# Kernel tuning notes

Measured on AMD Instinct MI355X. Metric: run time of the kernel, lower is better.

## Reference

```python
import jax, jax.numpy as jnp
import numpy as np

B, T, D, H = 2, 2048, 1024, 16
DK = D // H


def setup_inputs() -> dict:
    key = jax.random.key(0)
    ks = jax.random.split(key, 9)
    s = 1.0 / np.sqrt(D)
    x = jax.random.normal(ks[0], (B, T, D), dtype=jnp.float32)
    # causal mask (1 = attend, 0 = masked), broadcast over batch and heads
    mask = jnp.tril(jnp.ones((T, T), dtype=jnp.int32))[None, None, :, :]
    Wq = jax.random.uniform(ks[1], (D, D), jnp.float32, -s, s)
    bq = jax.random.uniform(ks[2], (D,), jnp.float32, -s, s)
    Wk = jax.random.uniform(ks[3], (D, D), jnp.float32, -s, s)
    bk = jax.random.uniform(ks[4], (D,), jnp.float32, -s, s)
    Wv = jax.random.uniform(ks[5], (D, D), jnp.float32, -s, s)
    bv = jax.random.uniform(ks[6], (D,), jnp.float32, -s, s)
    Wo = jax.random.uniform(ks[7], (D, D), jnp.float32, -s, s)
    bo = jax.random.uniform(ks[8], (D,), jnp.float32, -s, s)
    return {"x": x, "mask": mask, "Wq": Wq, "bq": bq, "Wk": Wk, "bk": bk,
            "Wv": Wv, "bv": bv, "Wo": Wo, "bo": bo}


def reference(x, mask, Wq, bq, Wk, bk, Wv, bv, Wo, bo):
    # nn.Linear: y = x @ W.T + b
    q = (x @ Wq.T + bq).reshape(B, T, H, DK).transpose(0, 2, 1, 3)  # [B,H,T,DK]
    k = (x @ Wk.T + bk).reshape(B, T, H, DK).transpose(0, 2, 1, 3)
    v = (x @ Wv.T + bv).reshape(B, T, H, DK).transpose(0, 2, 1, 3)
    scores = jnp.einsum('bhqd,bhkd->bhqk', q, k) / np.sqrt(DK).astype(np.float32)
    scores = jnp.where(mask == 0, -jnp.inf, scores)
    attn = jax.nn.softmax(scores, axis=-1)
    out = jnp.einsum('bhqk,bhkd->bhqd', attn, v)  # [B,H,T,DK]
    out = out.transpose(0, 2, 1, 3).reshape(B, T, D)
    return out @ Wo.T + bo
```

## Files before the change

kernel.cpp:

```cpp
#include <hip/hip_runtime.h>

typedef unsigned short u16;
typedef unsigned int u32;
typedef unsigned long long u64;
typedef __attribute__((ext_vector_type(8))) short short8;
typedef __attribute__((ext_vector_type(4))) float f32x4;

#define B_ 2
#define T_ 2048
#define H_ 16
#define DK_ 64
#define QSCALE 0.18033688011112042f

__device__ __forceinline__ u16 f2bf(float f){
  unsigned u = __float_as_uint(f);
  return (u16)((u + 0x7fffu + ((u >> 16) & 1u)) >> 16);
}

__device__ __forceinline__ u32 cvtpk(float lo, float hi){
  u32 r;
  asm("v_cvt_pk_bf16_f32 %0, %1, %2" : "=v"(r) : "v"(lo), "v"(hi));
  return r;
}

__device__ __forceinline__ short8 pack8(const f32x4 a, const f32x4 b){
  union { u32 u[4]; short8 s; } t;
  t.u[0] = cvtpk(a[0], a[1]); t.u[1] = cvtpk(a[2], a[3]);
  t.u[2] = cvtpk(b[0], b[1]); t.u[3] = cvtpk(b[2], b[3]);
  return t.s;
}

#define EXP2(x) __builtin_exp2f(x)

#if defined(__has_builtin)
#if __has_builtin(__builtin_amdgcn_global_load_lds)
#define HAS_GLLDS 1
#endif
#endif

#ifdef HAS_GLLDS
__device__ __forceinline__ void gl_lds16(const u16* g, u16* l){
  __builtin_amdgcn_global_load_lds(
      (__attribute__((address_space(1))) void*)(void*)g,
      (__attribute__((address_space(3))) void*)(void*)l, 16, 0, 0);
}
__device__ __forceinline__ void wait_vm4(){ asm volatile("s_waitcnt vmcnt(4)" ::: "memory"); }
__device__ __forceinline__ void wait_vm0(){ asm volatile("s_waitcnt vmcnt(0)" ::: "memory"); }
__device__ __forceinline__ void pipe_bar(){
  asm volatile("" ::: "memory");
  __builtin_amdgcn_s_barrier();
  asm volatile("" ::: "memory");
}
#else
__device__ __forceinline__ void wait_vm4(){}
__device__ __forceinline__ void wait_vm0(){}
__device__ __forceinline__ void pipe_bar(){ __syncthreads(); }
#endif

__global__ __launch_bounds__(256) void conv_all(
    const float* __restrict__ x, const float* __restrict__ wq, const float* __restrict__ wk,
    const float* __restrict__ wv, const float* __restrict__ wo,
    u16* __restrict__ xb, u16* __restrict__ wqb, u16* __restrict__ wkb,
    u16* __restrict__ wvb, u16* __restrict__ wob)
{
  int gid = blockIdx.x * 256 + threadIdx.x;
  const float* src; u16* dst; int off;
  if (gid < 1048576){ src = x; dst = xb; off = gid; }
  else {
    int t = gid - 1048576; int s = t >> 18; off = t & 262143;
    src = (s==0)?wq:((s==1)?wk:((s==2)?wv:wo));
    dst = (s==0)?wqb:((s==1)?wkb:((s==2)?wvb:wob));
  }
  float4 v = ((const float4*)src)[off];
  u64 r = (u64)f2bf(v.x) | ((u64)f2bf(v.y)<<16) | ((u64)f2bf(v.z)<<32) | ((u64)f2bf(v.w)<<48);
  ((u64*)dst)[off] = r;
}

template<int QKV>
__global__ __launch_bounds__(256, 3) void gemm_k5(
    const u16* __restrict__ A,
    const u16* __restrict__ W0, const u16* __restrict__ W1, const u16* __restrict__ W2,
    const float* __restrict__ b0, const float* __restrict__ b1, const float* __restrict__ b2,
    void* __restrict__ o0, void* __restrict__ o1, void* __restrict__ o2)
{
  __shared__ u16 As[3 * 4096];
  __shared__ u16 Bs[3 * 4096];
  const int tid = threadIdx.x;
  const int sel = QKV ? (blockIdx.x >> 3) : 0;
  const int n0 = (blockIdx.x & 7) * 128;
  const int m0 = blockIdx.y * 128;
  const u16* Bw = (sel==0)?W0:((sel==1)?W1:W2);
  const float* bias = (sel==0)?b0:((sel==1)?b1:b2);
  const int w = tid>>6, l = tid&63;
  const int lr = l&15, lg = l>>4;
  const int wm = (w&1)*64, wn = (w>>1)*64;
  const u16* Ab = A  + (size_t)m0*1024 + (size_t)(l>>2)*1024 + (l&3)*8;
  const u16* Bb = Bw + (size_t)n0*1024 + (size_t)(l>>2)*1024 + (l&3)*8;
  f32x4 acc[4][4] = {};

  auto STAGE = [&](int t, int pb){
#pragma unroll
    for (int i = 0; i < 2; ++i){
      int c = w*2 + i;
#ifdef HAS_GLLDS
      gl_lds16(Ab + (size_t)(16*c)*1024 + t*32, &As[pb*4096 + c*512]);
      gl_lds16(Bb + (size_t)(16*c)*1024 + t*32, &Bs[pb*4096 + c*512]);
#else
      *(uint4*)&As[pb*4096 + c*512 + l*8] = *(const uint4*)(Ab + (size_t)(16*c)*1024 + t*32);
      *(uint4*)&Bs[pb*4096 + c*512 + l*8] = *(const uint4*)(Bb + (size_t)(16*c)*1024 + t*32);
#endif
    }
  };

  STAGE(0, 0); STAGE(1, 1);
  wait_vm4();
  pipe_bar();
  for (int it = 0; it < 32; ++it){
    const int pb = it % 3;
    if (it < 30) STAGE(it + 2, (it + 2) % 3);
    short8 af[4], bf[4];
#pragma unroll
    for (int mi=0;mi<4;++mi) af[mi] = *(const short8*)&As[pb*4096 + (wm+16*mi+lr)*32 + 8*lg];
#pragma unroll
    for (int ni=0;ni<4;++ni) bf[ni] = *(const short8*)&Bs[pb*4096 + (wn+16*ni+lr)*32 + 8*lg];
#pragma unroll
    for (int mi=0;mi<4;++mi)
#pragma unroll
      for (int ni=0;ni<4;++ni)
        acc[mi][ni] = __builtin_amdgcn_mfma_f32_16x16x32_bf16(af[mi], bf[ni], acc[mi][ni], 0,0,0);
    if (it < 31){
      if (it < 30) wait_vm4();
      else         wait_vm0();
      pipe_bar();
    }
  }

  float bv[4];
#pragma unroll
  for (int ni=0;ni<4;++ni) bv[ni] = bias[n0+wn+16*ni+lr];
  void* C = QKV ? ((sel==0)?o0:((sel==1)?o1:o2)) : o0;
#pragma unroll
  for (int mi=0;mi<4;++mi)
#pragma unroll
    for (int r=0;r<4;++r){
      const int trow = m0 + wm + 16*mi + 4*lg + r;
#pragma unroll
      for (int ni=0;ni<4;++ni){
        float v = acc[mi][ni][r] + bv[ni];
        int n = n0 + wn + 16*ni + lr;
        if (!QKV){
          ((float*)C)[(size_t)trow*1024 + n] = v;
        } else if (sel == 0){
          ((u16*)C)[(size_t)trow*1024 + n] = f2bf(v * QSCALE);
        } else if (sel == 1){
          int nsw = (n & ~63) | ((n & 63) ^ ((trow & 7) << 3));
          ((u16*)C)[(size_t)trow*1024 + nsw] = f2bf(v);
        } else {
          ((u16*)C)[(size_t)trow*1024 + n] = f2bf(v);
        }
      }
    }
}

__global__ __launch_bounds__(256) void transpose_v_k(const u16* __restrict__ V,
                                                     u16* __restrict__ VT){
  __shared__ u16 L[64 * 72];
  const int tid = threadIdx.x;
  const int tc = blockIdx.x, h = blockIdx.y, b = blockIdx.z;
#pragma unroll
  for (int p = 0; p < 2; ++p){
    int row = (tid >> 3) + 32 * p, g = tid & 7;
    *(uint4*)&L[row * 72 + g * 8] =
        *(const uint4*)(V + ((size_t)(b * T_ + tc * 64 + row) * H_ + h) * DK_ + g * 8);
  }
  __syncthreads();
#pragma unroll
  for (int p = 0; p < 2; ++p){
    int d = tid >> 2, g8 = (tid & 3) + 4 * p;
    union { uint4 u; u16 s[8]; } tv;
#pragma unroll
    for (int i = 0; i < 8; ++i){
      int pp = 8 * g8 + i;
      int tl = 16 * (2 * ((pp >> 5) & 1) + ((pp >> 2) & 1)) + 4 * ((pp >> 3) & 3) + (pp & 3);
      tv.s[i] = L[tl * 72 + d];
    }
    *(uint4*)(VT + ((size_t)(b * H_ + h) * DK_ + d) * T_ + tc * 64 + ((8 * g8) ^ ((d & 7) << 3))) = tv.u;
  }
}

__global__ __launch_bounds__(256, 3) void attn_v6(
    const u16* __restrict__ Q, const u16* __restrict__ K,
    const u16* __restrict__ VT, u16* __restrict__ O)
{
  __shared__ u16 Ks[2][64 * 64];
  __shared__ u16 VTs[2][64 * 64];
  const int tid = threadIdx.x;
  const int w = tid >> 6, l = tid & 63;
  const int lr = l & 15, lg = l >> 4;
  const int h = blockIdx.y, b = blockIdx.z;
  const int qtb = (b == 0) ? blockIdx.x : (15 - blockIdx.x);
  const int q0 = qtb * 128;
  const int wrow0 = q0 + w * 32;
  const int sl_r = l >> 3, sl_c = (l & 7) * 8;
  const size_t kbase = ((size_t)(b * T_) * H_ + h) * DK_;
  const size_t vbase = (size_t)(b * H_ + h) * DK_ * (size_t)T_;

  auto STAGE = [&](int kt, int pb){
#pragma unroll
    for (int p = 0; p < 2; ++p){
      int r0 = 8 * w + 32 * p;
#ifdef HAS_GLLDS
      gl_lds16(K  + kbase + (size_t)(kt * 64 + r0 + sl_r) * 1024 + sl_c, &Ks[pb][r0 * 64]);
      gl_lds16(VT + vbase + (size_t)(r0 + sl_r) * T_ + kt * 64 + sl_c, &VTs[pb][r0 * 64]);
#else
      *(uint4*)&Ks[pb][(r0 + sl_r) * 64 + sl_c] =
          *(const uint4*)(K + kbase + (size_t)(kt * 64 + r0 + sl_r) * 1024 + sl_c);
      *(uint4*)&VTs[pb][(r0 + sl_r) * 64 + sl_c] =
          *(const uint4*)(VT + vbase + (size_t)(r0 + sl_r) * T_ + kt * 64 + sl_c);
#endif
    }
  };

  short8 qf[2][2];
#pragma unroll
  for (int mi = 0; mi < 2; ++mi)
#pragma unroll
    for (int s = 0; s < 2; ++s)
      qf[mi][s] = *(const short8*)(Q + kbase + (size_t)(wrow0 + 16 * mi + lr) * 1024 + s * 32 + 8 * lg);

  f32x4 acc[2][4] = {};
  float lsum[2] = {0.f, 0.f};
  const int ktend = 2 * qtb + 1;

  STAGE(0, 0);
  __syncthreads();
  for (int kt = 0; kt <= ktend; ++kt){
    const int pb = kt & 1;
    if (kt < ktend) STAGE(kt + 1, pb ^ 1);
    if (kt * 64 <= wrow0 + 31){
      short8 kf[4][2];
#pragma unroll
      for (int j0 = 0; j0 < 4; ++j0)
#pragma unroll
        for (int s = 0; s < 2; ++s)
          kf[j0][s] = *(const short8*)&Ks[pb][(j0 * 16 + lr) * 64 + (((4 * s + lg) ^ (lr & 7)) << 3)];
      short8 pf[2][2];
      const bool diag = (kt * 64 + 63 > wrow0);
      const int kc0 = kt * 64 + 4 * lg;
#pragma unroll
      for (int mi = 0; mi < 2; ++mi){
        f32x4 pr[4];
        float lacc = 0.f;
        const int qrow = wrow0 + 16 * mi + lr;
#pragma unroll
        for (int j0 = 0; j0 < 4; ++j0){
          f32x4 z = {};
          z = __builtin_amdgcn_mfma_f32_16x16x32_bf16(kf[j0][0], qf[mi][0], z, 0, 0, 0);
          z = __builtin_amdgcn_mfma_f32_16x16x32_bf16(kf[j0][1], qf[mi][1], z, 0, 0, 0);
#pragma unroll
          for (int r = 0; r < 4; ++r){
            float e = EXP2(z[r]);
            if (diag && (kc0 + 16 * j0 + r > qrow)) e = 0.f;
            pr[j0][r] = e;
            lacc += e;
          }
        }
        lsum[mi] += lacc;
        pf[mi][0] = pack8(pr[0], pr[1]);
        pf[mi][1] = pack8(pr[2], pr[3]);
      }
#pragma unroll
      for (int ks = 0; ks < 2; ++ks)
#pragma unroll
        for (int d0 = 0; d0 < 4; ++d0){
          short8 vf = *(const short8*)&VTs[pb][(d0 * 16 + lr) * 64 + (((4 * ks + lg) ^ (lr & 7)) << 3)];
          acc[0][d0] = __builtin_amdgcn_mfma_f32_16x16x32_bf16(pf[0][ks], vf, acc[0][d0], 0, 0, 0);
          acc[1][d0] = __builtin_amdgcn_mfma_f32_16x16x32_bf16(pf[1][ks], vf, acc[1][d0], 0, 0, 0);
        }
    }
    __syncthreads();
  }

#pragma unroll
  for (int mi = 0; mi < 2; ++mi){
    float v = lsum[mi];
    v += __shfl_xor(v, 16);
    v += __shfl_xor(v, 32);
    float inv = 1.0f / v;
    float invr[4];
#pragma unroll
    for (int r = 0; r < 4; ++r) invr[r] = __shfl(inv, 4 * lg + r);
#pragma unroll
    for (int d0 = 0; d0 < 4; ++d0)
#pragma unroll
      for (int r = 0; r < 4; ++r){
        float ov = acc[mi][d0][r] * invr[r];
        O[kbase + (size_t)(wrow0 + 16 * mi + 4 * lg + r) * 1024 + d0 * 16 + lr] = f2bf(ov);
      }
  }
}

extern "C" void kernel_launch(void* const* d_in, const int* in_sizes, int n_in,
                              void* d_out, int out_size, void* d_ws, size_t ws_size,
                              hipStream_t stream)
{
  const float* x  = (const float*)d_in[0];
  const float* Wq = (const float*)d_in[2];
  const float* bq = (const float*)d_in[3];
  const float* Wk = (const float*)d_in[4];
  const float* bk = (const float*)d_in[5];
  const float* Wv = (const float*)d_in[6];
  const float* bv = (const float*)d_in[7];
  const float* Wo = (const float*)d_in[8];
  const float* bo = (const float*)d_in[9];

  char* ws = (char*)d_ws;
  u16* xb  = (u16*)(ws + 0);
  u16* wqb = (u16*)(ws + 8388608);
  u16* wkb = (u16*)(ws + 10485760);
  u16* wvb = (u16*)(ws + 12582912);
  u16* wob = (u16*)(ws + 14680064);
  u16* qb  = (u16*)(ws + 16777216);
  u16* kb  = (u16*)(ws + 25165824);
  u16* vb  = (u16*)(ws + 33554432);
  u16* vtb = xb;
  u16* ab  = vb;

  conv_all<<<8192, 256, 0, stream>>>(x, Wq, Wk, Wv, Wo, xb, wqb, wkb, wvb, wob);

  gemm_k5<1><<<dim3(24, 32), 256, 0, stream>>>(
      xb, wqb, wkb, wvb, bq, bk, bv, (void*)qb, (void*)kb, (void*)vb);

  transpose_v_k<<<dim3(T_/64, H_, B_), 256, 0, stream>>>(vb, vtb);

  attn_v6<<<dim3(T_/128, H_, B_), 256, 0, stream>>>(qb, kb, vtb, ab);

  gemm_k5<0><<<dim3(8, 32), 256, 0, stream>>>(
      ab, wob, wob, wob, bo, bo, bo, d_out, d_out, d_out);
}
```

Baseline: 133.8 us.

## Widen attention KV tile to 128 keys and match V transpose layout

The attention kernel now processes 128 keys per iteration instead of 64. That halves the number of loop trips and barriers, and the K and V^T staging buffers grow to 128-wide double buffers. The V transpose kernel is rewritten for 128-token chunks to produce the matching swizzled layout, and occupancy drops from 3 to 2 blocks per CU. The per-wave skip of fully masked 64-key tiles is gone, so waves on the diagonal tile compute some fully masked work. EXP2 is also replaced by __expf of a scaled argument.

```diff
diff --git a/kernel.cpp b/kernel.cpp
--- a/kernel.cpp
+++ b/kernel.cpp
@@ -23,14 +23,14 @@
   return r;
 }
 
+#define EXP2(x) __expf(0.6931471805599453f * (x))
+
 __device__ __forceinline__ short8 pack8(const f32x4 a, const f32x4 b){
   union { u32 u[4]; short8 s; } t;
   t.u[0] = cvtpk(a[0], a[1]); t.u[1] = cvtpk(a[2], a[3]);
   t.u[2] = cvtpk(b[0], b[1]); t.u[3] = cvtpk(b[2], b[3]);
   return t.s;
 }
-
-#define EXP2(x) __builtin_exp2f(x)
 
 #if defined(__has_builtin)
 #if __has_builtin(__builtin_amdgcn_global_load_lds)
@@ -162,61 +162,69 @@
     }
 }
 
-__global__ __launch_bounds__(256) void transpose_v_k(const u16* __restrict__ V,
-                                                     u16* __restrict__ VT){
-  __shared__ u16 L[64 * 72];
+__global__ __launch_bounds__(256) void transpose_v128(const u16* __restrict__ V,
+                                                      u16* __restrict__ VT){
+  __shared__ u16 L[128 * 72];
   const int tid = threadIdx.x;
   const int tc = blockIdx.x, h = blockIdx.y, b = blockIdx.z;
 #pragma unroll
-  for (int p = 0; p < 2; ++p){
+  for (int p = 0; p < 4; ++p){
     int row = (tid >> 3) + 32 * p, g = tid & 7;
     *(uint4*)&L[row * 72 + g * 8] =
-        *(const uint4*)(V + ((size_t)(b * T_ + tc * 64 + row) * H_ + h) * DK_ + g * 8);
+        *(const uint4*)(V + ((size_t)(b * T_ + tc * 128 + row) * H_ + h) * DK_ + g * 8);
   }
   __syncthreads();
 #pragma unroll
-  for (int p = 0; p < 2; ++p){
+  for (int p = 0; p < 4; ++p){
     int d = tid >> 2, g8 = (tid & 3) + 4 * p;
     union { uint4 u; u16 s[8]; } tv;
 #pragma unroll
     for (int i = 0; i < 8; ++i){
       int pp = 8 * g8 + i;
-      int tl = 16 * (2 * ((pp >> 5) & 1) + ((pp >> 2) & 1)) + 4 * ((pp >> 3) & 3) + (pp & 3);
+      int tl = 32 * (pp >> 5) + 16 * ((pp >> 2) & 1) + 4 * ((pp >> 3) & 3) + (pp & 3);
       tv.s[i] = L[tl * 72 + d];
     }
-    *(uint4*)(VT + ((size_t)(b * H_ + h) * DK_ + d) * T_ + tc * 64 + ((8 * g8) ^ ((d & 7) << 3))) = tv.u;
-  }
-}
-
-__global__ __launch_bounds__(256, 3) void attn_v6(
+    *(uint4*)(VT + ((size_t)(b * H_ + h) * DK_ + d) * T_ + tc * 128 + ((8 * g8) ^ ((d & 7) << 3))) = tv.u;
+  }
+}
+
+__global__ __launch_bounds__(256, 2) void attn_v7(
     const u16* __restrict__ Q, const u16* __restrict__ K,
     const u16* __restrict__ VT, u16* __restrict__ O)
 {
-  __shared__ u16 Ks[2][64 * 64];
-  __shared__ u16 VTs[2][64 * 64];
+  __shared__ u16 Ks[2][128 * 64];
+  __shared__ u16 VTs[2][64 * 128];
   const int tid = threadIdx.x;
   const int w = tid >> 6, l = tid & 63;
   const int lr = l & 15, lg = l >> 4;
   const int h = blockIdx.y, b = blockIdx.z;
   const int qtb = (b == 0) ? blockIdx.x : (15 - blockIdx.x);
   const int q0 = qtb * 128;
-  const int wrow0 = q0 + w * 32;
-  const int sl_r = l >> 3, sl_c = (l & 7) * 8;
+  const int wrow0 = q0 + 32 * w;
   const size_t kbase = ((size_t)(b * T_) * H_ + h) * DK_;
   const size_t vbase = (size_t)(b * H_ + h) * DK_ * (size_t)T_;
 
   auto STAGE = [&](int kt, int pb){
 #pragma unroll
-    for (int p = 0; p < 2; ++p){
-      int r0 = 8 * w + 32 * p;
+    for (int p = 0; p < 4; ++p){
+      int kr0 = 32 * w + 8 * p;
 #ifdef HAS_GLLDS
-      gl_lds16(K  + kbase + (size_t)(kt * 64 + r0 + sl_r) * 1024 + sl_c, &Ks[pb][r0 * 64]);
-      gl_lds16(VT + vbase + (size_t)(r0 + sl_r) * T_ + kt * 64 + sl_c, &VTs[pb][r0 * 64]);
+      gl_lds16(K + kbase + (size_t)(kt * 128 + kr0 + (l >> 3)) * 1024 + (l & 7) * 8,
+               &Ks[pb][kr0 * 64]);
 #else
-      *(uint4*)&Ks[pb][(r0 + sl_r) * 64 + sl_c] =
-          *(const uint4*)(K + kbase + (size_t)(kt * 64 + r0 + sl_r) * 1024 + sl_c);
-      *(uint4*)&VTs[pb][(r0 + sl_r) * 64 + sl_c] =
-          *(const uint4*)(VT + vbase + (size_t)(r0 + sl_r) * T_ + kt * 64 + sl_c);
+      *(uint4*)&Ks[pb][(kr0 + (l >> 3)) * 64 + (l & 7) * 8] =
+          *(const uint4*)(K + kbase + (size_t)(kt * 128 + kr0 + (l >> 3)) * 1024 + (l & 7) * 8);
+#endif
+    }
+#pragma unroll
+    for (int p = 0; p < 4; ++p){
+      int dr0 = 16 * w + 4 * p;
+#ifdef HAS_GLLDS
+      gl_lds16(VT + vbase + (size_t)(dr0 + (l >> 4)) * T_ + kt * 128 + (l & 15) * 8,
+               &VTs[pb][dr0 * 128]);
+#else
+      *(uint4*)&VTs[pb][(dr0 + (l >> 4)) * 128 + (l & 15) * 8] =
+          *(const uint4*)(VT + vbase + (size_t)(dr0 + (l >> 4)) * T_ + kt * 128 + (l & 15) * 8);
 #endif
     }
   };
@@ -230,54 +238,55 @@
 
   f32x4 acc[2][4] = {};
   float lsum[2] = {0.f, 0.f};
-  const int ktend = 2 * qtb + 1;
+  const int ktend = qtb;
 
   STAGE(0, 0);
   __syncthreads();
   for (int kt = 0; kt <= ktend; ++kt){
     const int pb = kt & 1;
     if (kt < ktend) STAGE(kt + 1, pb ^ 1);
-    if (kt * 64 <= wrow0 + 31){
+    const bool diag = (kt == ktend);
+    short8 pf[2][4];
+#pragma unroll
+    for (int jh = 0; jh < 2; ++jh){
       short8 kf[4][2];
 #pragma unroll
-      for (int j0 = 0; j0 < 4; ++j0)
+      for (int j = 0; j < 4; ++j)
 #pragma unroll
         for (int s = 0; s < 2; ++s)
-          kf[j0][s] = *(const short8*)&Ks[pb][(j0 * 16 + lr) * 64 + (((4 * s + lg) ^ (lr & 7)) << 3)];
-      short8 pf[2][2];
-      const bool diag = (kt * 64 + 63 > wrow0);
-      const int kc0 = kt * 64 + 4 * lg;
+          kf[j][s] = *(const short8*)&Ks[pb][((4 * jh + j) * 16 + lr) * 64 + (((4 * s + lg) ^ (lr & 7)) << 3)];
 #pragma unroll
       for (int mi = 0; mi < 2; ++mi){
         f32x4 pr[4];
         float lacc = 0.f;
-        const int qrow = wrow0 + 16 * mi + lr;
-#pragma unroll
-        for (int j0 = 0; j0 < 4; ++j0){
+        const int lim = 32 * w + 16 * mi + lr;
+#pragma unroll
+        for (int j = 0; j < 4; ++j){
+          const int j0 = 4 * jh + j;
           f32x4 z = {};
-          z = __builtin_amdgcn_mfma_f32_16x16x32_bf16(kf[j0][0], qf[mi][0], z, 0, 0, 0);
-          z = __builtin_amdgcn_mfma_f32_16x16x32_bf16(kf[j0][1], qf[mi][1], z, 0, 0, 0);
+          z = __builtin_amdgcn_mfma_f32_16x16x32_bf16(kf[j][0], qf[mi][0], z, 0, 0, 0);
+          z = __builtin_amdgcn_mfma_f32_16x16x32_bf16(kf[j][1], qf[mi][1], z, 0, 0, 0);
 #pragma unroll
           for (int r = 0; r < 4; ++r){
             float e = EXP2(z[r]);
-            if (diag && (kc0 + 16 * j0 + r > qrow)) e = 0.f;
-            pr[j0][r] = e;
+            if (diag && (16 * j0 + 4 * lg + r > lim)) e = 0.f;
+            pr[j][r] = e;
             lacc += e;
           }
         }
         lsum[mi] += lacc;
-        pf[mi][0] = pack8(pr[0], pr[1]);
-        pf[mi][1] = pack8(pr[2], pr[3]);
+        pf[mi][2 * jh]     = pack8(pr[0], pr[1]);
+        pf[mi][2 * jh + 1] = pack8(pr[2], pr[3]);
       }
-#pragma unroll
-      for (int ks = 0; ks < 2; ++ks)
-#pragma unroll
-        for (int d0 = 0; d0 < 4; ++d0){
-          short8 vf = *(const short8*)&VTs[pb][(d0 * 16 + lr) * 64 + (((4 * ks + lg) ^ (lr & 7)) << 3)];
-          acc[0][d0] = __builtin_amdgcn_mfma_f32_16x16x32_bf16(pf[0][ks], vf, acc[0][d0], 0, 0, 0);
-          acc[1][d0] = __builtin_amdgcn_mfma_f32_16x16x32_bf16(pf[1][ks], vf, acc[1][d0], 0, 0, 0);
-        }
-    }
+    }
+#pragma unroll
+    for (int ks = 0; ks < 4; ++ks)
+#pragma unroll
+      for (int d0 = 0; d0 < 4; ++d0){
+        short8 vf = *(const short8*)&VTs[pb][(d0 * 16 + lr) * 128 + (((4 * ks + lg) ^ (lr & 7)) << 3)];
+        acc[0][d0] = __builtin_amdgcn_mfma_f32_16x16x32_bf16(pf[0][ks], vf, acc[0][d0], 0, 0, 0);
+        acc[1][d0] = __builtin_amdgcn_mfma_f32_16x16x32_bf16(pf[1][ks], vf, acc[1][d0], 0, 0, 0);
+      }
     __syncthreads();
   }
 
@@ -331,9 +340,9 @@
   gemm_k5<1><<<dim3(24, 32), 256, 0, stream>>>(
       xb, wqb, wkb, wvb, bq, bk, bv, (void*)qb, (void*)kb, (void*)vb);
 
-  transpose_v_k<<<dim3(T_/64, H_, B_), 256, 0, stream>>>(vb, vtb);
-
-  attn_v6<<<dim3(T_/128, H_, B_), 256, 0, stream>>>(qb, kb, vtb, ab);
+  transpose_v128<<<dim3(T_/128, H_, B_), 256, 0, stream>>>(vb, vtb);
+
+  attn_v7<<<dim3(T_/128, H_, B_), 256, 0, stream>>>(qb, kb, vtb, ab);
 
   gemm_k5<0><<<dim3(8, 32), 256, 0, stream>>>(
       ab, wob, wob, wob, bo, bo, bo, d_out, d_out, d_out);
```

After: 116.3 us. 1.15x faster.
